# Optimization experiments

Hardware: AMD Instinct MI355X
Metric: run time of the kernel (lower is better)

Reference implementation:

```python
import jax, jax.numpy as jnp
import numpy as np

EPS_BN = 1e-5
EPS_W = 1e-8


def _bn(x, g, b, m, v):
    # x: [B, N, C]; params: [C] (inference-mode batchnorm)
    return g * (x - m) * jax.lax.rsqrt(v + EPS_BN) + b


def setup_inputs() -> dict:
    key = jax.random.key(0)
    ks = jax.random.split(key, 24)
    B, N, S = 16, 4096, 1024
    C1, C2 = 128, 256            # points1 / points2 channels
    CIN, COUT = C1 + C2, 128     # in_channel, out_channel

    def w(k, shape, std=0.02):
        return (jax.random.normal(k, shape, jnp.float32) * std)

    def bn_params(k, c):
        k1, k2, k3, k4 = jax.random.split(k, 4)
        return (1.0 + 0.1 * jax.random.normal(k1, (c,), jnp.float32),  # gamma
                0.1 * jax.random.normal(k2, (c,), jnp.float32),        # beta
                0.1 * jax.random.normal(k3, (c,), jnp.float32),        # running mean
                0.5 + jax.random.uniform(k4, (c,), jnp.float32))       # running var

    fg, fb, fm, fv = bn_params(ks[4], COUT)
    g1, b1, m1, v1 = bn_params(ks[5], COUT)
    g2, b2, m2, v2 = bn_params(ks[6], COUT)
    return {
        "xyz1": jax.random.uniform(ks[0], (B, N, 3), jnp.float32),
        "xyz2": jax.random.uniform(ks[1], (B, S, 3), jnp.float32),
        "points1": jax.random.normal(ks[2], (B, C1, N), jnp.float32),
        "points2": jax.random.normal(ks[3], (B, C2, S), jnp.float32),
        "fuse_w": w(ks[7], (COUT, CIN)), "fuse_b": jnp.zeros((COUT,), jnp.float32),
        "fuse_g": fg, "fuse_beta": fb, "fuse_m": fm, "fuse_v": fv,
        "c1_w": w(ks[8], (COUT, COUT)), "c1_b": jnp.zeros((COUT,), jnp.float32),
        "bn1_g": g1, "bn1_b": b1, "bn1_m": m1, "bn1_v": v1,
        "c2_w": w(ks[9], (COUT, COUT)), "c2_b": jnp.zeros((COUT,), jnp.float32),
        "bn2_g": g2, "bn2_b": b2, "bn2_m": m2, "bn2_v": v2,
    }


def reference(xyz1, xyz2, points1, points2,
              fuse_w, fuse_b, fuse_g, fuse_beta, fuse_m, fuse_v,
              c1_w, c1_b, bn1_g, bn1_b, bn1_m, bn1_v,
              c2_w, c2_b, bn2_g, bn2_b, bn2_m, bn2_v):
    B, N, _ = xyz1.shape
    pts1 = jnp.swapaxes(points1, 1, 2)   # [B, N, C1]
    pts2 = jnp.swapaxes(points2, 1, 2)   # [B, S, C2]

    # squared pairwise distances [B, N, S]
    dists = (jnp.sum(xyz1 ** 2, -1)[:, :, None]
             + jnp.sum(xyz2 ** 2, -1)[:, None, :]
             - 2.0 * jnp.einsum('bnc,bsc->bns', xyz1, xyz2))

    # 3 nearest neighbors (smallest distances)
    neg_d3, idx = jax.lax.top_k(-dists, 3)          # [B, N, 3]
    d3 = -neg_d3
    recip = 1.0 / (d3 + EPS_W)
    weight = recip / jnp.sum(recip, axis=2, keepdims=True)  # [B, N, 3]

    gathered = jax.vmap(lambda p, i: p[i])(pts2, idx)        # [B, N, 3, C2]
    interp = jnp.sum(gathered * weight[..., None], axis=2)   # [B, N, C2]

    x = jnp.concatenate([pts1, interp], axis=-1)             # [B, N, CIN]

    # fuse: 1x1 conv + BN + ReLU
    x = jax.nn.relu(_bn(jnp.einsum('bnc,oc->bno', x, fuse_w) + fuse_b,
                        fuse_g, fuse_beta, fuse_m, fuse_v))

    # residual block: conv-BN-ReLU -> conv-BN, add skip, ReLU
    h = jax.nn.relu(_bn(jnp.einsum('bnc,oc->bno', x, c1_w) + c1_b,
                        bn1_g, bn1_b, bn1_m, bn1_v))
    y = _bn(jnp.einsum('bnc,oc->bno', h, c2_w) + c2_b,
            bn2_g, bn2_b, bn2_m, bn2_v)
    out = jax.nn.relu(y + x)                                 # [B, N, COUT]
    return jnp.swapaxes(out, 1, 2)                           # [B, COUT, N]
```

## Files before the change

### kernel.cpp

```cpp
#include <hip/hip_runtime.h>
#include <hip/hip_bf16.h>

#define BB 16
#define NN 4096
#define SS 1024
#define C1 128
#define C2 256
#define CIN 384
#define CO 128

#define KCH 16
#define SCH (SS / KCH)

typedef __bf16 bf16x8 __attribute__((ext_vector_type(8)));
typedef float f32x4 __attribute__((ext_vector_type(4)));

__global__ __launch_bounds__(256) void knn_part_kernel(
    const float* __restrict__ xyz1, const float* __restrict__ xyz2,
    float4* __restrict__ pd4, int4* __restrict__ pi4)
{
    __shared__ float4 pts[SCH];
    const int b = blockIdx.z;
    const int ch = blockIdx.y;
    const float* p2 = xyz2 + ((size_t)b * SS + (size_t)ch * SCH) * 3;
    for (int i = threadIdx.x; i < SCH; i += 256) {
        float x = p2[i * 3 + 0], y = p2[i * 3 + 1], z = p2[i * 3 + 2];
        pts[i] = make_float4(x, y, z, x * x + y * y + z * z);
    }
    __syncthreads();

    const int n = blockIdx.x * 256 + threadIdx.x;
    const float* p1 = xyz1 + ((size_t)b * NN + n) * 3;
    const float x = p1[0], y = p1[1], z = p1[2];
    const float s1 = x * x + y * y + z * z;

    float d0 = 3.4e38f, d1 = 3.4e38f, d2 = 3.4e38f, d3 = 3.4e38f;
    int i0 = 0, i1 = 0, i2 = 0, i3 = 0;
    const int sbase = ch * SCH;
    #pragma unroll 4
    for (int sl = 0; sl < SCH; ++sl) {
        float4 p = pts[sl];
        float d = s1 + p.w - 2.0f * (x * p.x + y * p.y + z * p.z);
        int s = sbase + sl;
        bool lt0 = d < d0, lt1 = d < d1, lt2 = d < d2, lt3 = d < d3;
        float nd3 = lt2 ? d2 : (lt3 ? d : d3); int ni3 = lt2 ? i2 : (lt3 ? s : i3);
        float nd2 = lt1 ? d1 : (lt2 ? d : d2); int ni2 = lt1 ? i1 : (lt2 ? s : i2);
        float nd1 = lt0 ? d0 : (lt1 ? d : d1); int ni1 = lt0 ? i0 : (lt1 ? s : i1);
        d0 = lt0 ? d : d0;                     i0 = lt0 ? s : i0;
        d1 = nd1; i1 = ni1; d2 = nd2; i2 = ni2; d3 = nd3; i3 = ni3;
    }
    size_t o = ((size_t)b * NN + n) * KCH + ch;
    pd4[o] = make_float4(d0, d1, d2, d3);
    pi4[o] = make_int4(i0, i1, i2, i3);
}

__global__ __launch_bounds__(256) void knn_merge_kernel(
    const float4* __restrict__ pd4, const int4* __restrict__ pi4,
    int* __restrict__ idx4, float* __restrict__ w4)
{
    const int n = blockIdx.x * 256 + threadIdx.x;
    const int b = blockIdx.y;
    const size_t o = ((size_t)b * NN + n) * KCH;

    float d0 = 3.4e38f, d1 = 3.4e38f, d2 = 3.4e38f, d3 = 3.4e38f;
    int i0 = 0, i1 = 0, i2 = 0, i3 = 0;
    #pragma unroll
    for (int ch = 0; ch < KCH; ++ch) {
        float4 pd = pd4[o + ch];
        int4 pi = pi4[o + ch];
        float cd[4] = { pd.x, pd.y, pd.z, pd.w };
        int   ci[4] = { pi.x, pi.y, pi.z, pi.w };
        #pragma unroll
        for (int k = 0; k < 4; ++k) {
            float d = cd[k]; int s = ci[k];
            bool lt0 = d < d0, lt1 = d < d1, lt2 = d < d2, lt3 = d < d3;
            float nd3 = lt2 ? d2 : (lt3 ? d : d3); int ni3 = lt2 ? i2 : (lt3 ? s : i3);
            float nd2 = lt1 ? d1 : (lt2 ? d : d2); int ni2 = lt1 ? i1 : (lt2 ? s : i2);
            float nd1 = lt0 ? d0 : (lt1 ? d : d1); int ni1 = lt0 ? i0 : (lt1 ? s : i1);
            d0 = lt0 ? d : d0;                     i0 = lt0 ? s : i0;
            d1 = nd1; i1 = ni1; d2 = nd2; i2 = ni2; d3 = nd3; i3 = ni3;
        }
    }
    float r0 = 1.0f / (d0 + 1e-8f);
    float r1 = 1.0f / (d1 + 1e-8f);
    float r2 = 1.0f / (d2 + 1e-8f);
    float rs = r0 + r1 + r2;
    bool tie = (d2 == d3);
    size_t base = ((size_t)b * NN + n) * 4;
    idx4[base + 0] = i0; idx4[base + 1] = i1;
    idx4[base + 2] = i2; idx4[base + 3] = i3;
    w4[base + 0] = r0 / rs; w4[base + 1] = r1 / rs;
    w4[base + 2] = r2 / rs; w4[base + 3] = tie ? -1.0f : 0.0f;
}

__global__ __launch_bounds__(256) void p2t_kernel(
    const float* __restrict__ p2, float* __restrict__ p2t)
{
    __shared__ float tile[64][65];
    const int b = blockIdx.z;
    const int s0 = blockIdx.x * 64, c0 = blockIdx.y * 64;
    for (int i = threadIdx.x; i < 64 * 64; i += 256) {
        int s = i & 63, c = i >> 6;
        tile[c][s] = p2[((size_t)b * C2 + c0 + c) * SS + s0 + s];
    }
    __syncthreads();
    for (int i = threadIdx.x; i < 64 * 64; i += 256) {
        int c = i & 63, s = i >> 6;
        p2t[((size_t)b * SS + s0 + s) * C2 + c0 + c] = tile[c][s];
    }
}

__global__ __launch_bounds__(256) void wprep_kernel(
    const float* __restrict__ fw, const float* __restrict__ w1,
    const float* __restrict__ w2,
    __bf16* __restrict__ Whf, __bf16* __restrict__ Wlf,
    __bf16* __restrict__ Wh1, __bf16* __restrict__ Wl1,
    __bf16* __restrict__ Wh2, __bf16* __restrict__ Wl2)
{
    int t = blockIdx.x * 256 + threadIdx.x;
    float v; __bf16 *oh, *ol; int idx;
    if (t < 49152)      { idx = t;         v = fw[idx]; oh = Whf; ol = Wlf; }
    else if (t < 65536) { idx = t - 49152; v = w1[idx]; oh = Wh1; ol = Wl1; }
    else                { idx = t - 65536; v = w2[idx]; oh = Wh2; ol = Wl2; }
    __bf16 h = (__bf16)v;
    oh[idx] = h; ol[idx] = (__bf16)(v - (float)h);
}

__global__ __launch_bounds__(256) void tie_eval_kernel(
    const float* __restrict__ p2t, const float* __restrict__ points1,
    const int* __restrict__ idx4, float* __restrict__ w4,
    const float* __restrict__ fw, const float* __restrict__ fb,
    const float* __restrict__ fg, const float* __restrict__ fbt,
    const float* __restrict__ fm, const float* __restrict__ fv,
    const float* __restrict__ w1m, const float* __restrict__ b1,
    const float* __restrict__ g1, const float* __restrict__ bt1,
    const float* __restrict__ m1, const float* __restrict__ v1,
    const float* __restrict__ w2m, const float* __restrict__ b2,
    const float* __restrict__ g2, const float* __restrict__ bt2,
    const float* __restrict__ m2, const float* __restrict__ v2)
{
    __shared__ float Xs[4][2][CIN];
    __shared__ float XT[4][2][CO];
    __shared__ float Hs[4][2][CO];
    const int wave = threadIdx.x >> 6, lane = threadIdx.x & 63;
    const int n = blockIdx.x * 4 + wave;
    const int b = blockIdx.y;
    const size_t base = ((size_t)b * NN + n) * 4;
    if (w4[base + 3] != -1.0f) return;

    const int i0 = idx4[base + 0], i1 = idx4[base + 1];
    const int i2 = idx4[base + 2], i3 = idx4[base + 3];
    const float w0 = w4[base + 0], w1 = w4[base + 1], w2 = w4[base + 2];
    const float* P = p2t + (size_t)b * SS * C2;

    for (int c = lane; c < C1; c += 64) {
        float v = points1[((size_t)b * C1 + c) * NN + n];
        Xs[wave][0][c] = v; Xs[wave][1][c] = v;
    }
    for (int c = lane; c < C2; c += 64) {
        float f0 = P[(size_t)i0 * C2 + c], f1 = P[(size_t)i1 * C2 + c];
        float f2 = P[(size_t)i2 * C2 + c], f3 = P[(size_t)i3 * C2 + c];
        float bs = w0 * f0 + w1 * f1;
        Xs[wave][0][C1 + c] = bs + w2 * f2;
        Xs[wave][1][C1 + c] = bs + w2 * f3;
    }
    #pragma unroll
    for (int k = 0; k < 2; ++k) {
        int oc = lane + 64 * k;
        float alo = fb[oc], ahi = fb[oc];
        for (int c = 0; c < CIN; ++c) {
            float wv = fw[(size_t)oc * CIN + c];
            alo += wv * Xs[wave][0][c];
            ahi += wv * Xs[wave][1][c];
        }
        float s = fg[oc] * (1.0f / sqrtf(fv[oc] + 1e-5f));
        XT[wave][0][oc] = fmaxf(s * (alo - fm[oc]) + fbt[oc], 0.0f);
        XT[wave][1][oc] = fmaxf(s * (ahi - fm[oc]) + fbt[oc], 0.0f);
    }
    #pragma unroll
    for (int k = 0; k < 2; ++k) {
        int oc = lane + 64 * k;
        float alo = b1[oc], ahi = b1[oc];
        for (int c = 0; c < CO; ++c) {
            float wv = w1m[(size_t)oc * CO + c];
            alo += wv * XT[wave][0][c];
            ahi += wv * XT[wave][1][c];
        }
        float s = g1[oc] * (1.0f / sqrtf(v1[oc] + 1e-5f));
        Hs[wave][0][oc] = fmaxf(s * (alo - m1[oc]) + bt1[oc], 0.0f);
        Hs[wave][1][oc] = fmaxf(s * (ahi - m1[oc]) + bt1[oc], 0.0f);
    }
    float e = 0.0f;
    #pragma unroll
    for (int k = 0; k < 2; ++k) {
        int oc = lane + 64 * k;
        float alo = b2[oc], ahi = b2[oc];
        for (int c = 0; c < CO; ++c) {
            float wv = w2m[(size_t)oc * CO + c];
            alo += wv * Hs[wave][0][c];
            ahi += wv * Hs[wave][1][c];
        }
        float s = g2[oc] * (1.0f / sqrtf(v2[oc] + 1e-5f));
        float olo = fmaxf(s * (alo - m2[oc]) + bt2[oc] + XT[wave][0][oc], 0.0f);
        float ohi = fmaxf(s * (alo - m2[oc]) + bt2[oc] + XT[wave][1][oc], 0.0f) - fmaxf(s * (alo - m2[oc]) + bt2[oc] + XT[wave][1][oc], 0.0f) + fmaxf(s * (ahi - m2[oc]) + bt2[oc] + XT[wave][1][oc], 0.0f);
        e = fmaxf(e, fabsf(olo - ohi));
    }
    for (int off = 32; off; off >>= 1) e = fmaxf(e, __shfl_xor(e, off));
    if (lane == 0) {
        if (e > 0.085f) { w4[base + 3] = 0.0f; }
        else { w4[base + 2] = 0.5f * w2; w4[base + 3] = 0.5f * w2; }
    }
}

__global__ __launch_bounds__(512) void gemm1f_kernel(
    const float* __restrict__ points1, const float* __restrict__ p2t,
    const int* __restrict__ idx4, const float* __restrict__ w4,
    const __bf16* __restrict__ Wh, const __bf16* __restrict__ Wl,
    const float* __restrict__ cb,  const float* __restrict__ gg,
    const float* __restrict__ bbta, const float* __restrict__ mm,
    const float* __restrict__ vv,
    __bf16* __restrict__ outh, __bf16* __restrict__ outl)
{
    __shared__ __attribute__((aligned(16))) __bf16 wls_h[128 * 40];
    __shared__ __attribute__((aligned(16))) __bf16 wls_l[128 * 40];
    __shared__ float s_s[128], s_t[128];
    const int tid = threadIdx.x;
    if (tid < 128) {
        float s = gg[tid] * (1.0f / sqrtf(vv[tid] + 1e-5f));
        float t = (cb[tid] - mm[tid]) * s + bbta[tid];
        s_s[tid] = s; s_t[tid] = t;
    }
    const int bid = (blockIdx.x & 7) * 64 + (blockIdx.x >> 3);
    const int b = bid >> 5;
    const int nbase = (bid & 31) * 128;
    const int wave = tid >> 6, lane = tid & 63;
    const int m = lane & 15, q = lane >> 4;

    const size_t pa = (size_t)b * NN + nbase + wave * 16 + m;
    const int4   ia4 = *(const int4*)&idx4[pa * 4];
    const float4 wa4 = *(const float4*)&w4[pa * 4];
    const float* P = p2t + (size_t)b * SS * C2;

    f32x4 acc[8] = {};
    const int wrow = tid >> 2, wseg = tid & 3;

    for (int kk = 0; kk < CIN; kk += 32) {
        __syncthreads();
        {
            size_t g = (size_t)wrow * CIN + kk + wseg * 8;
            int lo = wrow * 40 + wseg * 8;
            *(uint4*)&wls_h[lo] = *(const uint4*)&Wh[g];
            *(uint4*)&wls_l[lo] = *(const uint4*)&Wl[g];
        }
        __syncthreads();

        bf16x8 ah0, al0;
        if (kk < C1) {
            const float* p1 = points1 + ((size_t)b * C1 + kk + q * 8) * NN
                            + nbase + wave * 16 + m;
            #pragma unroll
            for (int j = 0; j < 8; ++j) {
                float v = p1[(size_t)j * NN];
                __bf16 h = (__bf16)v;
                ah0[j] = h; al0[j] = (__bf16)(v - (float)h);
            }
        } else {
            const int c0 = kk - C1 + q * 8;
            const float* g0 = P + (size_t)ia4.x * C2 + c0;
            const float* g1 = P + (size_t)ia4.y * C2 + c0;
            const float* g2 = P + (size_t)ia4.z * C2 + c0;
            const float* g3 = P + (size_t)ia4.w * C2 + c0;
            #pragma unroll
            for (int hh = 0; hh < 2; ++hh) {
                float4 f0 = *(const float4*)(g0 + hh * 4);
                float4 f1 = *(const float4*)(g1 + hh * 4);
                float4 f2 = *(const float4*)(g2 + hh * 4);
                float4 f3 = *(const float4*)(g3 + hh * 4);
                float v0 = wa4.x * f0.x + wa4.y * f1.x + wa4.z * f2.x + wa4.w * f3.x;
                float v1 = wa4.x * f0.y + wa4.y * f1.y + wa4.z * f2.y + wa4.w * f3.y;
                float v2 = wa4.x * f0.z + wa4.y * f1.z + wa4.z * f2.z + wa4.w * f3.z;
                float v3 = wa4.x * f0.w + wa4.y * f1.w + wa4.z * f2.w + wa4.w * f3.w;
                __bf16 h0 = (__bf16)v0, h1 = (__bf16)v1, h2 = (__bf16)v2, h3 = (__bf16)v3;
                ah0[hh * 4 + 0] = h0; al0[hh * 4 + 0] = (__bf16)(v0 - (float)h0);
                ah0[hh * 4 + 1] = h1; al0[hh * 4 + 1] = (__bf16)(v1 - (float)h1);
                ah0[hh * 4 + 2] = h2; al0[hh * 4 + 2] = (__bf16)(v2 - (float)h2);
                ah0[hh * 4 + 3] = h3; al0[hh * 4 + 3] = (__bf16)(v3 - (float)h3);
            }
        }

        #pragma unroll
        for (int ot = 0; ot < 8; ++ot) {
            bf16x8 bh = *(const bf16x8*)&wls_h[(ot * 16 + m) * 40 + q * 8];
            bf16x8 bl = *(const bf16x8*)&wls_l[(ot * 16 + m) * 40 + q * 8];
            acc[ot] = __builtin_amdgcn_mfma_f32_16x16x32_bf16(ah0, bh, acc[ot], 0, 0, 0);
            acc[ot] = __builtin_amdgcn_mfma_f32_16x16x32_bf16(al0, bh, acc[ot], 0, 0, 0);
            acc[ot] = __builtin_amdgcn_mfma_f32_16x16x32_bf16(ah0, bl, acc[ot], 0, 0, 0);
        }
    }

    const size_t r0 = (size_t)bid * 128 + wave * 16;
    #pragma unroll
    for (int ot = 0; ot < 8; ++ot) {
        int col = ot * 16 + m;
        float sc = s_s[col], sh = s_t[col];
        #pragma unroll
        for (int r = 0; r < 4; ++r) {
            size_t row = r0 + q * 4 + r;
            float val = fmaxf(acc[ot][r] * sc + sh, 0.0f);
            __bf16 h = (__bf16)val;
            outh[row * 128 + col] = h;
            outl[row * 128 + col] = (__bf16)(val - (float)h);
        }
    }
}

template<int K, int MODE>
__global__ __launch_bounds__(512) void gemm_bn_kernel(
    const __bf16* __restrict__ Ah, const __bf16* __restrict__ Al,
    const __bf16* __restrict__ Wh, const __bf16* __restrict__ Wl,
    const float* __restrict__ cb,  const float* __restrict__ gg,
    const float* __restrict__ bbta, const float* __restrict__ mm,
    const float* __restrict__ vv,
    const __bf16* __restrict__ skiph, const __bf16* __restrict__ skipl,
    __bf16* __restrict__ outh, __bf16* __restrict__ outl,
    float* __restrict__ outf)
{
    __shared__ __attribute__((aligned(16))) __bf16 wls_h[128 * 40];
    __shared__ __attribute__((aligned(16))) __bf16 wls_l[128 * 40];
    __shared__ float s_s[128], s_t[128];
    __shared__ float tile[32][132];
    const int tid = threadIdx.x;
    if (tid < 128) {
        float s = gg[tid] * (1.0f / sqrtf(vv[tid] + 1e-5f));
        float t = (cb[tid] - mm[tid]) * s + bbta[tid];
        s_s[tid] = s; s_t[tid] = t;
    }
    const int wave = tid >> 6, lane = tid & 63;
    const int m = lane & 15, q = lane >> 4;
    const size_t r0 = (size_t)blockIdx.x * 128 + wave * 16;

    f32x4 acc[8] = {};
    const __bf16* pAh = Ah + (r0 + m) * (size_t)K + q * 8;
    const __bf16* pAl = Al + (r0 + m) * (size_t)K + q * 8;

    const int wrow = tid >> 2, wseg = tid & 3;
    for (int kk = 0; kk < K; kk += 32) {
        __syncthreads();
        {
            size_t g = (size_t)wrow * K + kk + wseg * 8;
            int lo = wrow * 40 + wseg * 8;
            *(uint4*)&wls_h[lo] = *(const uint4*)&Wh[g];
            *(uint4*)&wls_l[lo] = *(const uint4*)&Wl[g];
        }
        __syncthreads();
        bf16x8 ah0 = *(const bf16x8*)(pAh + kk);
        bf16x8 al0 = *(const bf16x8*)(pAl + kk);
        #pragma unroll
        for (int ot = 0; ot < 8; ++ot) {
            bf16x8 bh = *(const bf16x8*)&wls_h[(ot * 16 + m) * 40 + q * 8];
            bf16x8 bl = *(const bf16x8*)&wls_l[(ot * 16 + m) * 40 + q * 8];
            acc[ot] = __builtin_amdgcn_mfma_f32_16x16x32_bf16(ah0, bh, acc[ot], 0, 0, 0);
            acc[ot] = __builtin_amdgcn_mfma_f32_16x16x32_bf16(al0, bh, acc[ot], 0, 0, 0);
            acc[ot] = __builtin_amdgcn_mfma_f32_16x16x32_bf16(ah0, bl, acc[ot], 0, 0, 0);
        }
    }

    if (MODE == 0) {
        #pragma unroll
        for (int ot = 0; ot < 8; ++ot) {
            int col = ot * 16 + m;
            float sc = s_s[col], sh = s_t[col];
            #pragma unroll
            for (int r = 0; r < 4; ++r) {
                size_t row = r0 + q * 4 + r;
                float val = fmaxf(acc[ot][r] * sc + sh, 0.0f);
                __bf16 h = (__bf16)val;
                outh[row * 128 + col] = h;
                outl[row * 128 + col] = (__bf16)(val - (float)h);
            }
        }
    } else {
        const int bidx = (int)(((size_t)blockIdx.x * 128) >> 12);
        const int nbase = (int)(((size_t)blockIdx.x * 128) & 4095);
        for (int cc = 0; cc < 4; ++cc) {
            __syncthreads();
            #pragma unroll
            for (int oo = 0; oo < 2; ++oo) {
                int ot = cc * 2 + oo;
                int col = ot * 16 + m;
                float sc = s_s[col], sh = s_t[col];
                #pragma unroll
                for (int r = 0; r < 4; ++r) {
                    int lrow = wave * 16 + q * 4 + r;
                    size_t row = (size_t)blockIdx.x * 128 + lrow;
                    float val = acc[ot][r] * sc + sh;
                    val += (float)skiph[row * 128 + col] + (float)skipl[row * 128 + col];
                    val = fmaxf(val, 0.0f);
                    tile[oo * 16 + m][lrow] = val;
                }
            }
            __syncthreads();
            for (int c2 = tid >> 7; c2 < 32; c2 += 4) {
                int nn_ = tid & 127;
                outf[((size_t)bidx * 128 + cc * 32 + c2) * NN + nbase + nn_] = tile[c2][nn_];
            }
        }
    }
}

extern "C" void kernel_launch(void* const* d_in, const int* in_sizes, int n_in,
                              void* d_out, int out_size, void* d_ws, size_t ws_size,
                              hipStream_t stream) {
    const float* xyz1    = (const float*)d_in[0];
    const float* xyz2    = (const float*)d_in[1];
    const float* points1 = (const float*)d_in[2];
    const float* points2 = (const float*)d_in[3];
    const float* fuse_w  = (const float*)d_in[4];
    const float* fuse_b  = (const float*)d_in[5];
    const float* fuse_g  = (const float*)d_in[6];
    const float* fuse_bt = (const float*)d_in[7];
    const float* fuse_m  = (const float*)d_in[8];
    const float* fuse_v  = (const float*)d_in[9];
    const float* c1_w    = (const float*)d_in[10];
    const float* c1_b    = (const float*)d_in[11];
    const float* bn1_g   = (const float*)d_in[12];
    const float* bn1_b   = (const float*)d_in[13];
    const float* bn1_m   = (const float*)d_in[14];
    const float* bn1_v   = (const float*)d_in[15];
    const float* c2_w    = (const float*)d_in[16];
    const float* c2_b    = (const float*)d_in[17];
    const float* bn2_g   = (const float*)d_in[18];
    const float* bn2_b   = (const float*)d_in[19];
    const float* bn2_m   = (const float*)d_in[20];
    const float* bn2_v   = (const float*)d_in[21];

    char* ws = (char*)d_ws;
    int*    idx4 = (int*)(ws);
    float*  w4   = (float*)(ws + 1048576);
    float*  p2t  = (float*)(ws + 2097152);
    __bf16* Y0h  = (__bf16*)(ws + 119537664);
    __bf16* Y0l  = (__bf16*)(ws + 136314880);
    __bf16* Hh   = (__bf16*)(ws + 153092096);
    __bf16* Hl   = (__bf16*)(ws + 169869312);
    __bf16* Whf  = (__bf16*)(ws + 186646528);
    __bf16* Wlf  = (__bf16*)(ws + 186744832);
    __bf16* Wh1  = (__bf16*)(ws + 186843136);
    __bf16* Wl1  = (__bf16*)(ws + 186875904);
    __bf16* Wh2  = (__bf16*)(ws + 186908672);
    __bf16* Wl2  = (__bf16*)(ws + 186941440);

    float4* pd4 = (float4*)(ws + 18874368);
    int4*   pi4 = (int4*)(ws + 18874368 + 16777216);

    knn_part_kernel<<<dim3(NN / 256, KCH, BB), 256, 0, stream>>>(xyz1, xyz2, pd4, pi4);
    knn_merge_kernel<<<dim3(NN / 256, BB), 256, 0, stream>>>(pd4, pi4, idx4, w4);
    p2t_kernel<<<dim3(SS / 64, C2 / 64, BB), 256, 0, stream>>>(points2, p2t);
    wprep_kernel<<<320, 256, 0, stream>>>(fuse_w, c1_w, c2_w,
                                          Whf, Wlf, Wh1, Wl1, Wh2, Wl2);
    tie_eval_kernel<<<dim3(NN / 4, BB), 256, 0, stream>>>(
        p2t, points1, idx4, w4,
        fuse_w, fuse_b, fuse_g, fuse_bt, fuse_m, fuse_v,
        c1_w, c1_b, bn1_g, bn1_b, bn1_m, bn1_v,
        c2_w, c2_b, bn2_g, bn2_b, bn2_m, bn2_v);

    const int gblocks = (BB * NN) / 128;
    gemm1f_kernel<<<gblocks, 512, 0, stream>>>(
        points1, p2t, idx4, w4, Whf, Wlf,
        fuse_b, fuse_g, fuse_bt, fuse_m, fuse_v, Y0h, Y0l);
    gemm_bn_kernel<CO, 0><<<gblocks, 512, 0, stream>>>(
        Y0h, Y0l, Wh1, Wl1, c1_b, bn1_g, bn1_b, bn1_m, bn1_v,
        nullptr, nullptr, Hh, Hl, nullptr);
    gemm_bn_kernel<CO, 1><<<gblocks, 512, 0, stream>>>(
        Hh, Hl, Wh2, Wl2, c2_b, bn2_g, bn2_b, bn2_m, bn2_v,
        Y0h, Y0l, nullptr, nullptr, (float*)d_out);
}
```

Before: 315.1 us.

## Split fuse GEMM output columns across blocks and preload full-K weight slice

```diff
diff --git a/kernel.cpp b/kernel.cpp
--- a/kernel.cpp
+++ b/kernel.cpp
@@ -221,18 +221,35 @@
     const float* __restrict__ vv,
     __bf16* __restrict__ outh, __bf16* __restrict__ outl)
 {
-    __shared__ __attribute__((aligned(16))) __bf16 wls_h[128 * 40];
-    __shared__ __attribute__((aligned(16))) __bf16 wls_l[128 * 40];
-    __shared__ float s_s[128], s_t[128];
+    #define WST 392
+    __shared__ __attribute__((aligned(16))) __bf16 wls_h[32 * WST];
+    __shared__ __attribute__((aligned(16))) __bf16 wls_l[32 * WST];
+    __shared__ float s_s[32], s_t[32];
     const int tid = threadIdx.x;
-    if (tid < 128) {
-        float s = gg[tid] * (1.0f / sqrtf(vv[tid] + 1e-5f));
-        float t = (cb[tid] - mm[tid]) * s + bbta[tid];
-        s_s[tid] = s; s_t[tid] = t;
-    }
-    const int bid = (blockIdx.x & 7) * 64 + (blockIdx.x >> 3);
-    const int b = bid >> 5;
-    const int nbase = (bid & 31) * 128;
+
+    const int swz = (blockIdx.x & 7) * 256 + (blockIdx.x >> 3);
+    const int colq = swz & 3;
+    const int rowblk = swz >> 2;
+    const int b = rowblk >> 5;
+    const int nbase = (rowblk & 31) * 128;
+
+    #pragma unroll
+    for (int k = 0; k < 3; ++k) {
+        int i = tid + k * 512;
+        int col = i / 48, oct = i % 48;
+        size_t g = (size_t)(colq * 32 + col) * CIN + oct * 8;
+        int lo = col * WST + oct * 8;
+        *(uint4*)&wls_h[lo] = *(const uint4*)&Wh[g];
+        *(uint4*)&wls_l[lo] = *(const uint4*)&Wl[g];
+    }
+    if (tid < 32) {
+        int oc = colq * 32 + tid;
+        float s = gg[oc] * (1.0f / sqrtf(vv[oc] + 1e-5f));
+        s_s[tid] = s;
+        s_t[tid] = (cb[oc] - mm[oc]) * s + bbta[oc];
+    }
+    __syncthreads();
+
     const int wave = tid >> 6, lane = tid & 63;
     const int m = lane & 15, q = lane >> 4;
 
@@ -241,68 +258,67 @@
     const float4 wa4 = *(const float4*)&w4[pa * 4];
     const float* P = p2t + (size_t)b * SS * C2;
 
-    f32x4 acc[8] = {};
-    const int wrow = tid >> 2, wseg = tid & 3;
-
-    for (int kk = 0; kk < CIN; kk += 32) {
-        __syncthreads();
-        {
-            size_t g = (size_t)wrow * CIN + kk + wseg * 8;
-            int lo = wrow * 40 + wseg * 8;
-            *(uint4*)&wls_h[lo] = *(const uint4*)&Wh[g];
-            *(uint4*)&wls_l[lo] = *(const uint4*)&Wl[g];
-        }
-        __syncthreads();
-
+    f32x4 acc[2] = {};
+
+    for (int kk = 0; kk < C1; kk += 32) {
         bf16x8 ah0, al0;
-        if (kk < C1) {
-            const float* p1 = points1 + ((size_t)b * C1 + kk + q * 8) * NN
-                            + nbase + wave * 16 + m;
-            #pragma unroll
-            for (int j = 0; j < 8; ++j) {
-                float v = p1[(size_t)j * NN];
-                __bf16 h = (__bf16)v;
-                ah0[j] = h; al0[j] = (__bf16)(v - (float)h);
-            }
-        } else {
-            const int c0 = kk - C1 + q * 8;
-            const float* g0 = P + (size_t)ia4.x * C2 + c0;
-            const float* g1 = P + (size_t)ia4.y * C2 + c0;
-            const float* g2 = P + (size_t)ia4.z * C2 + c0;
-            const float* g3 = P + (size_t)ia4.w * C2 + c0;
-            #pragma unroll
-            for (int hh = 0; hh < 2; ++hh) {
-                float4 f0 = *(const float4*)(g0 + hh * 4);
-                float4 f1 = *(const float4*)(g1 + hh * 4);
-                float4 f2 = *(const float4*)(g2 + hh * 4);
-                float4 f3 = *(const float4*)(g3 + hh * 4);
-                float v0 = wa4.x * f0.x + wa4.y * f1.x + wa4.z * f2.x + wa4.w * f3.x;
-                float v1 = wa4.x * f0.y + wa4.y * f1.y + wa4.z * f2.y + wa4.w * f3.y;
-                float v2 = wa4.x * f0.z + wa4.y * f1.z + wa4.z * f2.z + wa4.w * f3.z;
-                float v3 = wa4.x * f0.w + wa4.y * f1.w + wa4.z * f2.w + wa4.w * f3.w;
-                __bf16 h0 = (__bf16)v0, h1 = (__bf16)v1, h2 = (__bf16)v2, h3 = (__bf16)v3;
-                ah0[hh * 4 + 0] = h0; al0[hh * 4 + 0] = (__bf16)(v0 - (float)h0);
-                ah0[hh * 4 + 1] = h1; al0[hh * 4 + 1] = (__bf16)(v1 - (float)h1);
-                ah0[hh * 4 + 2] = h2; al0[hh * 4 + 2] = (__bf16)(v2 - (float)h2);
-                ah0[hh * 4 + 3] = h3; al0[hh * 4 + 3] = (__bf16)(v3 - (float)h3);
-            }
-        }
-
-        #pragma unroll
-        for (int ot = 0; ot < 8; ++ot) {
-            bf16x8 bh = *(const bf16x8*)&wls_h[(ot * 16 + m) * 40 + q * 8];
-            bf16x8 bl = *(const bf16x8*)&wls_l[(ot * 16 + m) * 40 + q * 8];
+        const float* p1 = points1 + ((size_t)b * C1 + kk + q * 8) * NN
+                        + nbase + wave * 16 + m;
+        #pragma unroll
+        for (int j = 0; j < 8; ++j) {
+            float v = p1[(size_t)j * NN];
+            __bf16 h = (__bf16)v;
+            ah0[j] = h; al0[j] = (__bf16)(v - (float)h);
+        }
+        #pragma unroll
+        for (int ot = 0; ot < 2; ++ot) {
+            bf16x8 bh = *(const bf16x8*)&wls_h[(ot * 16 + m) * WST + kk + q * 8];
+            bf16x8 bl = *(const bf16x8*)&wls_l[(ot * 16 + m) * WST + kk + q * 8];
             acc[ot] = __builtin_amdgcn_mfma_f32_16x16x32_bf16(ah0, bh, acc[ot], 0, 0, 0);
             acc[ot] = __builtin_amdgcn_mfma_f32_16x16x32_bf16(al0, bh, acc[ot], 0, 0, 0);
             acc[ot] = __builtin_amdgcn_mfma_f32_16x16x32_bf16(ah0, bl, acc[ot], 0, 0, 0);
         }
     }
 
-    const size_t r0 = (size_t)bid * 128 + wave * 16;
-    #pragma unroll
-    for (int ot = 0; ot < 8; ++ot) {
-        int col = ot * 16 + m;
-        float sc = s_s[col], sh = s_t[col];
+    for (int kk = C1; kk < CIN; kk += 32) {
+        bf16x8 ah0, al0;
+        const int c0 = kk - C1 + q * 8;
+        const float* g0 = P + (size_t)ia4.x * C2 + c0;
+        const float* g1 = P + (size_t)ia4.y * C2 + c0;
+        const float* g2 = P + (size_t)ia4.z * C2 + c0;
+        const float* g3 = P + (size_t)ia4.w * C2 + c0;
+        #pragma unroll
+        for (int hh = 0; hh < 2; ++hh) {
+            float4 f0 = *(const float4*)(g0 + hh * 4);
+            float4 f1 = *(const float4*)(g1 + hh * 4);
+            float4 f2 = *(const float4*)(g2 + hh * 4);
+            float4 f3 = *(const float4*)(g3 + hh * 4);
+            float v0 = wa4.x * f0.x + wa4.y * f1.x + wa4.z * f2.x + wa4.w * f3.x;
+            float v1 = wa4.x * f0.y + wa4.y * f1.y + wa4.z * f2.y + wa4.w * f3.y;
+            float v2 = wa4.x * f0.z + wa4.y * f1.z + wa4.z * f2.z + wa4.w * f3.z;
+            float v3 = wa4.x * f0.w + wa4.y * f1.w + wa4.z * f2.w + wa4.w * f3.w;
+            __bf16 h0 = (__bf16)v0, h1 = (__bf16)v1, h2 = (__bf16)v2, h3 = (__bf16)v3;
+            ah0[hh * 4 + 0] = h0; al0[hh * 4 + 0] = (__bf16)(v0 - (float)h0);
+            ah0[hh * 4 + 1] = h1; al0[hh * 4 + 1] = (__bf16)(v1 - (float)h1);
+            ah0[hh * 4 + 2] = h2; al0[hh * 4 + 2] = (__bf16)(v2 - (float)h2);
+            ah0[hh * 4 + 3] = h3; al0[hh * 4 + 3] = (__bf16)(v3 - (float)h3);
+        }
+        #pragma unroll
+        for (int ot = 0; ot < 2; ++ot) {
+            bf16x8 bh = *(const bf16x8*)&wls_h[(ot * 16 + m) * WST + kk + q * 8];
+            bf16x8 bl = *(const bf16x8*)&wls_l[(ot * 16 + m) * WST + kk + q * 8];
+            acc[ot] = __builtin_amdgcn_mfma_f32_16x16x32_bf16(ah0, bh, acc[ot], 0, 0, 0);
+            acc[ot] = __builtin_amdgcn_mfma_f32_16x16x32_bf16(al0, bh, acc[ot], 0, 0, 0);
+            acc[ot] = __builtin_amdgcn_mfma_f32_16x16x32_bf16(ah0, bl, acc[ot], 0, 0, 0);
+        }
+    }
+
+    const size_t r0 = (size_t)rowblk * 128 + wave * 16;
+    #pragma unroll
+    for (int ot = 0; ot < 2; ++ot) {
+        int lc = ot * 16 + m;
+        int col = colq * 32 + lc;
+        float sc = s_s[lc], sh = s_t[lc];
         #pragma unroll
         for (int r = 0; r < 4; ++r) {
             size_t row = r0 + q * 4 + r;
@@ -312,6 +328,7 @@
             outl[row * 128 + col] = (__bf16)(val - (float)h);
         }
     }
+    #undef WST
 }
 
 template<int K, int MODE>
@@ -464,7 +481,7 @@
         c2_w, c2_b, bn2_g, bn2_b, bn2_m, bn2_v);
 
     const int gblocks = (BB * NN) / 128;
-    gemm1f_kernel<<<gblocks, 512, 0, stream>>>(
+    gemm1f_kernel<<<2048, 512, 0, stream>>>(
         points1, p2t, idx4, w4, Whf, Wlf,
         fuse_b, fuse_g, fuse_bt, fuse_m, fuse_v, Y0h, Y0l);
     gemm_bn_kernel<CO, 0><<<gblocks, 512, 0, stream>>>(
```

Result: slower. 396.2 us (+25.7%).

## Split GEMM output columns across blocks, preload full weight half, swizzle block order

Applied to the files above, without the earlier changes.

```diff
diff --git a/kernel.cpp b/kernel.cpp
--- a/kernel.cpp
+++ b/kernel.cpp
@@ -202,7 +202,7 @@
         }
         float s = g2[oc] * (1.0f / sqrtf(v2[oc] + 1e-5f));
         float olo = fmaxf(s * (alo - m2[oc]) + bt2[oc] + XT[wave][0][oc], 0.0f);
-        float ohi = fmaxf(s * (alo - m2[oc]) + bt2[oc] + XT[wave][1][oc], 0.0f) - fmaxf(s * (alo - m2[oc]) + bt2[oc] + XT[wave][1][oc], 0.0f) + fmaxf(s * (ahi - m2[oc]) + bt2[oc] + XT[wave][1][oc], 0.0f);
+        float ohi = fmaxf(s * (ahi - m2[oc]) + bt2[oc] + XT[wave][1][oc], 0.0f);
         e = fmaxf(e, fabsf(olo - ohi));
     }
     for (int off = 32; off; off >>= 1) e = fmaxf(e, __shfl_xor(e, off));
@@ -325,40 +325,48 @@
     __bf16* __restrict__ outh, __bf16* __restrict__ outl,
     float* __restrict__ outf)
 {
-    __shared__ __attribute__((aligned(16))) __bf16 wls_h[128 * 40];
-    __shared__ __attribute__((aligned(16))) __bf16 wls_l[128 * 40];
-    __shared__ float s_s[128], s_t[128];
+    #define WSTB 136
+    __shared__ __attribute__((aligned(16))) __bf16 wls_h[64 * WSTB];
+    __shared__ __attribute__((aligned(16))) __bf16 wls_l[64 * WSTB];
+    __shared__ float s_s[64], s_t[64];
     __shared__ float tile[32][132];
     const int tid = threadIdx.x;
-    if (tid < 128) {
-        float s = gg[tid] * (1.0f / sqrtf(vv[tid] + 1e-5f));
-        float t = (cb[tid] - mm[tid]) * s + bbta[tid];
-        s_s[tid] = s; s_t[tid] = t;
-    }
+
+    const int swz = (blockIdx.x & 7) * 128 + (blockIdx.x >> 3);
+    const int colh = swz & 1;
+    const int rowblk = swz >> 1;
+    const size_t row0 = (size_t)rowblk * 128;
+
+    for (int i = tid; i < 64 * (K / 8); i += 512) {
+        int col = i / (K / 8), ch = i % (K / 8);
+        size_t g = (size_t)(colh * 64 + col) * K + ch * 8;
+        int lo = col * WSTB + ch * 8;
+        *(uint4*)&wls_h[lo] = *(const uint4*)&Wh[g];
+        *(uint4*)&wls_l[lo] = *(const uint4*)&Wl[g];
+    }
+    if (tid < 64) {
+        int oc = colh * 64 + tid;
+        float s = gg[oc] * (1.0f / sqrtf(vv[oc] + 1e-5f));
+        s_s[tid] = s;
+        s_t[tid] = (cb[oc] - mm[oc]) * s + bbta[oc];
+    }
+    __syncthreads();
+
     const int wave = tid >> 6, lane = tid & 63;
     const int m = lane & 15, q = lane >> 4;
-    const size_t r0 = (size_t)blockIdx.x * 128 + wave * 16;
-
-    f32x4 acc[8] = {};
+    const size_t r0 = row0 + wave * 16;
+
+    f32x4 acc[4] = {};
     const __bf16* pAh = Ah + (r0 + m) * (size_t)K + q * 8;
     const __bf16* pAl = Al + (r0 + m) * (size_t)K + q * 8;
 
-    const int wrow = tid >> 2, wseg = tid & 3;
     for (int kk = 0; kk < K; kk += 32) {
-        __syncthreads();
-        {
-            size_t g = (size_t)wrow * K + kk + wseg * 8;
-            int lo = wrow * 40 + wseg * 8;
-            *(uint4*)&wls_h[lo] = *(const uint4*)&Wh[g];
-            *(uint4*)&wls_l[lo] = *(const uint4*)&Wl[g];
-        }
-        __syncthreads();
         bf16x8 ah0 = *(const bf16x8*)(pAh + kk);
         bf16x8 al0 = *(const bf16x8*)(pAl + kk);
         #pragma unroll
-        for (int ot = 0; ot < 8; ++ot) {
-            bf16x8 bh = *(const bf16x8*)&wls_h[(ot * 16 + m) * 40 + q * 8];
-            bf16x8 bl = *(const bf16x8*)&wls_l[(ot * 16 + m) * 40 + q * 8];
+        for (int ot = 0; ot < 4; ++ot) {
+            bf16x8 bh = *(const bf16x8*)&wls_h[(ot * 16 + m) * WSTB + kk + q * 8];
+            bf16x8 bl = *(const bf16x8*)&wls_l[(ot * 16 + m) * WSTB + kk + q * 8];
             acc[ot] = __builtin_amdgcn_mfma_f32_16x16x32_bf16(ah0, bh, acc[ot], 0, 0, 0);
             acc[ot] = __builtin_amdgcn_mfma_f32_16x16x32_bf16(al0, bh, acc[ot], 0, 0, 0);
             acc[ot] = __builtin_amdgcn_mfma_f32_16x16x32_bf16(ah0, bl, acc[ot], 0, 0, 0);
@@ -367,9 +375,10 @@
 
     if (MODE == 0) {
         #pragma unroll
-        for (int ot = 0; ot < 8; ++ot) {
-            int col = ot * 16 + m;
-            float sc = s_s[col], sh = s_t[col];
+        for (int ot = 0; ot < 4; ++ot) {
+            int lc = ot * 16 + m;
+            int col = colh * 64 + lc;
+            float sc = s_s[lc], sh = s_t[lc];
             #pragma unroll
             for (int r = 0; r < 4; ++r) {
                 size_t row = r0 + q * 4 + r;
@@ -380,19 +389,20 @@
             }
         }
     } else {
-        const int bidx = (int)(((size_t)blockIdx.x * 128) >> 12);
-        const int nbase = (int)(((size_t)blockIdx.x * 128) & 4095);
-        for (int cc = 0; cc < 4; ++cc) {
+        const int bidx = (int)(row0 >> 12);
+        const int nbase = (int)(row0 & 4095);
+        for (int cc = 0; cc < 2; ++cc) {
             __syncthreads();
             #pragma unroll
             for (int oo = 0; oo < 2; ++oo) {
                 int ot = cc * 2 + oo;
-                int col = ot * 16 + m;
-                float sc = s_s[col], sh = s_t[col];
+                int lc = ot * 16 + m;
+                int col = colh * 64 + lc;
+                float sc = s_s[lc], sh = s_t[lc];
                 #pragma unroll
                 for (int r = 0; r < 4; ++r) {
                     int lrow = wave * 16 + q * 4 + r;
-                    size_t row = (size_t)blockIdx.x * 128 + lrow;
+                    size_t row = row0 + lrow;
                     float val = acc[ot][r] * sc + sh;
                     val += (float)skiph[row * 128 + col] + (float)skipl[row * 128 + col];
                     val = fmaxf(val, 0.0f);
@@ -402,10 +412,12 @@
             __syncthreads();
             for (int c2 = tid >> 7; c2 < 32; c2 += 4) {
                 int nn_ = tid & 127;
-                outf[((size_t)bidx * 128 + cc * 32 + c2) * NN + nbase + nn_] = tile[c2][nn_];
+                outf[((size_t)bidx * 128 + colh * 64 + cc * 32 + c2) * NN + nbase + nn_]
+                    = tile[c2][nn_];
             }
         }
     }
+    #undef WSTB
 }
 
 extern "C" void kernel_launch(void* const* d_in, const int* in_sizes, int n_in,
@@ -467,10 +479,10 @@
     gemm1f_kernel<<<gblocks, 512, 0, stream>>>(
         points1, p2t, idx4, w4, Whf, Wlf,
         fuse_b, fuse_g, fuse_bt, fuse_m, fuse_v, Y0h, Y0l);
-    gemm_bn_kernel<CO, 0><<<gblocks, 512, 0, stream>>>(
+    gemm_bn_kernel<CO, 0><<<1024, 512, 0, stream>>>(
         Y0h, Y0l, Wh1, Wl1, c1_b, bn1_g, bn1_b, bn1_m, bn1_v,
         nullptr, nullptr, Hh, Hl, nullptr);
-    gemm_bn_kernel<CO, 1><<<gblocks, 512, 0, stream>>>(
+    gemm_bn_kernel<CO, 1><<<1024, 512, 0, stream>>>(
         Hh, Hl, Wh2, Wl2, c2_b, bn2_g, bn2_b, bn2_m, bn2_v,
         Y0h, Y0l, nullptr, nullptr, (float*)d_out);
 }
```

After: 312.3 us. About the same (-0.9%).
